# Performance work log

Measured on AMD Instinct MI355X. Metric: run time of the kernel, lower is better.

## Reference

```python
import jax, jax.numpy as jnp
import numpy as np

# ---- constants from the source module ----
N_SAMPLES = 2 ** 15          # exp.n_samples
N_FRAMES = 128
N_HARMONICS = 8
N_EVENTS = 8
FILT_SIZE = 16               # freq_domain_filter_size
N_NOTES = 128                # len(scale)
NYQ = 22050.0 / 2.0          # samplerate nyquist
MIN_F0 = 40.0 / NYQ
F0_SPAN = (3000.0 / NYQ) - MIN_F0
MIN_RES = 0.5
RES_SPAN = 1.0 - MIN_RES
B_EVENTS = 128               # batch(16) * n_events(8)

# packed layout (build_param_slices order):
SL_F0 = slice(0, N_NOTES)                       # 0:128
SL_AMP = slice(N_NOTES + N_FRAMES, N_NOTES + 2 * N_FRAMES)   # 256:384
SL_HAMP = slice(N_NOTES + 2 * N_FRAMES, N_NOTES + 2 * N_FRAMES + N_HARMONICS)  # 384:392
SL_HDEC = slice(N_NOTES + 2 * N_FRAMES + N_HARMONICS, N_NOTES + 2 * N_FRAMES + 2 * N_HARMONICS)  # 392:400
SL_FENV = slice(N_NOTES + 2 * N_FRAMES + 2 * N_HARMONICS, N_NOTES + 2 * N_FRAMES + 2 * N_HARMONICS + FILT_SIZE)  # 400:416


def interp_linear(x, out_size):
    """F.interpolate(..., mode='linear', align_corners=False) on last dim of [B,C,L]."""
    L = x.shape[-1]
    scale = L / out_size
    coords = (jnp.arange(out_size, dtype=x.dtype) + 0.5) * scale - 0.5
    coords = jnp.clip(coords, 0.0, L - 1)
    i0 = jnp.floor(coords).astype(jnp.int32)
    i1 = jnp.minimum(i0 + 1, L - 1)
    w = coords - i0.astype(x.dtype)
    return x[..., i0] * (1.0 - w) + x[..., i1] * w


def setup_inputs() -> dict:
    key = jax.random.key(0)
    k1, k2 = jax.random.split(key)
    packed = jax.random.uniform(k1, (B_EVENTS, N_NOTES + 2 * N_FRAMES + 2 * N_HARMONICS + FILT_SIZE), dtype=jnp.float32)
    # musical-scale center frequencies, normalized by nyquist (geometric 20..3000 Hz)
    hz = 20.0 * (3000.0 / 20.0) ** (np.arange(N_NOTES) / (N_NOTES - 1))
    frequencies = jnp.asarray(hz / NYQ, dtype=jnp.float32)
    global_amp = jnp.full((1,), 5000.0, dtype=jnp.float32)
    osc_amp = jnp.full((1,), 50.0, dtype=jnp.float32)
    noise = jax.random.uniform(k2, (B_EVENTS, 1, N_SAMPLES), dtype=jnp.float32, minval=-1.0, maxval=1.0)
    return {"packed": packed, "frequencies": frequencies, "global_amp": global_amp,
            "osc_amp": osc_amp, "noise": noise}


def reference(packed, frequencies, global_amp, osc_amp, noise):
    B = packed.shape[0]
    # ---- f0 (discrete): softmax over notes, expectation, squared, repeated per frame ----
    f0_scalar = jax.nn.softmax(packed[:, SL_F0], axis=-1) @ frequencies          # [B]
    f0 = (f0_scalar ** 2)[:, None, None] * jnp.ones((1, 1, N_FRAMES), packed.dtype)  # [B,1,F]
    f0 = f0 * NYQ
    f0 = MIN_F0 + f0 * F0_SPAN
    # (the torch line `f0 + f0 + f0_fine` has no assignment -> no effect; f0_fine unused)

    # ---- oscillator bank ----
    harm_factors = jnp.arange(1, N_HARMONICS + 1, dtype=packed.dtype)
    osc = f0 * harm_factors[None, :, None]                      # [B,H,F]
    radians = osc / NYQ * jnp.pi
    radians = jnp.where(radians >= jnp.pi, 0.0, radians)
    radians = interp_linear(radians, N_SAMPLES)                  # [B,H,S]
    osc_bank = jnp.sin(jnp.cumsum(radians, axis=-1)) * osc_amp   # [B,H,S]

    # ---- per-harmonic amplitude recurrence (scan over frames) ----
    harm_decay = MIN_RES + packed[:, SL_HDEC] * RES_SPAN         # [B,H]
    harm_amp = packed[:, SL_HAMP]                                # [B,H]
    amp = packed[:, SL_AMP][:, None, :] * 2.0 - 1.0              # [B,1,F]

    def step(current, amp_i):                                    # current [B,H], amp_i [B,1]
        cur = jnp.maximum(current + amp_i * harm_amp, 0.0)       # clamp(0, inf)
        return cur * harm_decay, cur

    amp_frames = jnp.moveaxis(amp[:, 0, :], 1, 0)[:, :, None]    # [F,B,1]
    _, res = jax.lax.scan(step, jnp.zeros((B, N_HARMONICS), packed.dtype), amp_frames)
    res = jnp.moveaxis(res, 0, 2)                                # [B,H,F]
    res_full = interp_linear(res, N_SAMPLES)                     # [B,H,S]

    # ---- FFT-filtered noise ----
    amp_full = interp_linear(amp, N_SAMPLES)                     # [B,1,S]
    nf = packed[:, SL_FENV][:, None, :]                          # [B,1,16]
    nf = interp_linear(nf, N_SAMPLES // 2)
    nf = jnp.pad(nf, ((0, 0), (0, 0), (0, 1)))                   # [B,1,S//2+1]
    noise_scaled = noise * global_amp
    spec = jnp.fft.rfft(noise_scaled, axis=-1, norm='ortho')
    filt = spec * nf
    noise_out = jnp.fft.irfft(filt, n=N_SAMPLES, axis=-1, norm='ortho')
    noise_out = noise_out * jnp.where(amp_full >= 0, amp_full, 0.2 * amp_full)  # leaky_relu(0.2)

    # ---- combine ----
    x = res_full * osc_bank                                      # [B,H,S]
    x = noise_out / N_HARMONICS + x                              # broadcast [B,1,S]
    x = x.reshape(-1, N_EVENTS, N_HARMONICS, N_SAMPLES)
    x = jnp.sum(x, axis=(1, 2)).reshape(-1, 1, N_SAMPLES)        # [batch,1,S]
    return x
```

## Files before the change

kernel.cpp:

```cpp
#include <hip/hip_runtime.h>
#include <math.h>

#define PCK_STRIDE 416
#define N_SAMPLES  32768
#define FFT_M      16384
#define B_EVENTS   128
#define N_GROUPS   16
#define NT         1024
#define PI_F 3.14159265358979323846f
#define RT2H 0.70710678118654752f

#define MAP(i) ((i) + (((i) >> 5) << 2))
#define LDS_N  18432

__device__ inline float filt_at(const float* __restrict__ f, int k) {
    if (k >= FFT_M) return 0.0f;
    float c = ((float)k + 0.5f) * (1.0f / 1024.0f) - 0.5f;
    c = fminf(fmaxf(c, 0.0f), 15.0f);
    int i0 = (int)floorf(c);
    int i1 = min(i0 + 1, 15);
    float w = c - (float)i0;
    return f[i0] * (1.0f - w) + f[i1] * w;
}

template<int L>
__device__ inline void r4_dif_stage(float* re, float* im, int tid) {
    constexpr int q = L >> 2;
    constexpr float ang = -6.28318530717958647692f / (float)L;
    #pragma unroll 1
    for (int s = 0; s < (FFT_M / 4) / NT; ++s) {
        int m = tid + s * NT;
        int t = m & (q - 1);
        int i0 = ((m & ~(q - 1)) << 2) | t;
        int ia = MAP(i0), ib = MAP(i0 + q), ic = MAP(i0 + 2 * q), id = MAP(i0 + 3 * q);
        float ar = re[ia], ai = im[ia];
        float br = re[ib], bi = im[ib];
        float cr = re[ic], ci = im[ic];
        float dr = re[id], di = im[id];
        float s1, c1; __sincosf(ang * (float)t, &s1, &c1);
        float c2 = c1 * c1 - s1 * s1, s2 = 2.0f * c1 * s1;
        float c3 = c2 * c1 - s2 * s1, s3 = c2 * s1 + s2 * c1;
        float s0r = ar + cr, s0i = ai + ci;
        float t1r = br + dr, t1i = bi + di;
        float d0r = ar - cr, d0i = ai - ci;
        float d1r = br - dr, d1i = bi - di;
        re[ia] = s0r + t1r; im[ia] = s0i + t1i;
        float er = s0r - t1r, ei = s0i - t1i;
        re[ib] = er * c2 - ei * s2; im[ib] = er * s2 + ei * c2;
        float fr = d0r + d1i, fi = d0i - d1r;
        re[ic] = fr * c1 - fi * s1; im[ic] = fr * s1 + fi * c1;
        float gr = d0r - d1i, gi = d0i + d1r;
        re[id] = gr * c3 - gi * s3; im[id] = gr * s3 + gi * c3;
    }
    __syncthreads();
}

template<int L>
__device__ inline void r4_dit_stage(float* re, float* im, int tid) {
    constexpr int q = L >> 2;
    constexpr float ang = 6.28318530717958647692f / (float)L;
    #pragma unroll 1
    for (int s = 0; s < (FFT_M / 4) / NT; ++s) {
        int m = tid + s * NT;
        int t = m & (q - 1);
        int i0 = ((m & ~(q - 1)) << 2) | t;
        int ia = MAP(i0), ib = MAP(i0 + q), ic = MAP(i0 + 2 * q), id = MAP(i0 + 3 * q);
        float ar = re[ia], ai = im[ia];
        float br = re[ib], bi = im[ib];
        float cr = re[ic], ci = im[ic];
        float dr = re[id], di = im[id];
        float s1, c1; __sincosf(ang * (float)t, &s1, &c1);
        float c2 = c1 * c1 - s1 * s1, s2 = 2.0f * c1 * s1;
        float tbr = br * c2 - bi * s2, tbi = br * s2 + bi * c2;
        float tdr = dr * c2 - di * s2, tdi = dr * s2 + di * c2;
        float B0r = ar + tbr, B0i = ai + tbi;
        float B1r = ar - tbr, B1i = ai - tbi;
        float B2r = cr + tdr, B2i = ci + tdi;
        float B3r = cr - tdr, B3i = ci - tdi;
        float t0r = B2r * c1 - B2i * s1, t0i = B2r * s1 + B2i * c1;
        float t1r = -B3r * s1 - B3i * c1, t1i = B3r * c1 - B3i * s1;
        re[ia] = B0r + t0r; im[ia] = B0i + t0i;
        re[ib] = B1r + t1r; im[ib] = B1i + t1i;
        re[ic] = B0r - t0r; im[ic] = B0i - t0i;
        re[id] = B1r - t1r; im[id] = B1i - t1i;
    }
    __syncthreads();
}

__global__ __launch_bounds__(NT)
void fft_filter_kernel(
    const float* __restrict__ noise, const float* __restrict__ packed,
    const float* __restrict__ gamp, float* __restrict__ noise_out,
    const float* __restrict__ freqs, float* __restrict__ rW, float* __restrict__ res)
{
    extern __shared__ float smem[];
    float* re = smem;
    float* im = smem + LDS_N;
    float* filt = smem + 2 * LDS_N;
    const int b = blockIdx.x;
    const int tid = threadIdx.x;
    const float g = gamp[0];

    const float2* nz = (const float2*)(noise + (size_t)b * N_SAMPLES);
    #pragma unroll 1
    for (int s = 0; s < 8192 / NT; ++s) {
        int j = tid + s * NT;
        float2 v0 = nz[j];
        float2 v1 = nz[j + 8192];
        float ur = v0.x * g, ui = v0.y * g;
        float wr = v1.x * g, wi = v1.y * g;
        float s1, c1; __sincosf((-PI_F / 8192.0f) * (float)j, &s1, &c1);
        int a0 = MAP(j), a1 = MAP(j + 8192);
        re[a0] = ur + wr; im[a0] = ui + wi;
        float dr = ur - wr, di = ui - wi;
        re[a1] = dr * c1 - di * s1;
        im[a1] = dr * s1 + di * c1;
    }
    if (tid >= 64 && tid < 80) filt[tid - 64] = packed[b * PCK_STRIDE + 400 + (tid - 64)];

    if (tid < 64) {
        const float* row = packed + b * PCK_STRIDE;
        float n0 = row[tid], n1 = row[tid + 64];
        float fq0 = freqs[tid], fq1 = freqs[tid + 64];
        float mx = fmaxf(n0, n1);
        #pragma unroll
        for (int off = 32; off >= 1; off >>= 1) mx = fmaxf(mx, __shfl_xor(mx, off));
        float e0 = __expf(n0 - mx), e1 = __expf(n1 - mx);
        float den = e0 + e1, num = e0 * fq0 + e1 * fq1;
        #pragma unroll
        for (int off = 32; off >= 1; off >>= 1) {
            den += __shfl_xor(den, off);
            num += __shfl_xor(num, off);
        }
        float ampA = row[256 + tid] * 2.0f - 1.0f;
        float ampB = row[320 + tid] * 2.0f - 1.0f;
        int h = tid & 7;
        float ha = row[384 + h];
        float hd = 0.5f + row[392 + h] * 0.5f;
        const float MIN_F0 = 40.0f / 11025.0f;
        const float F0_SPAN = 3000.0f / 11025.0f - 40.0f / 11025.0f;
        float f0s = num / den;
        float f0 = MIN_F0 + f0s * f0s * 11025.0f * F0_SPAN;
        float r = f0 * (float)(h + 1) * (PI_F / 11025.0f);
        if (r >= PI_F) r = 0.0f;
        if (tid < 8) rW[b * 8 + tid] = r;
        float cur = 0.0f;
        float* rr = res + (b * 8 + h) * 128;
        for (int f = 0; f < 64; ++f) {
            float av = __shfl(ampA, f);
            float c = fmaxf(cur + av * ha, 0.0f);
            if (tid < 8) rr[f] = c;
            cur = c * hd;
        }
        for (int f = 0; f < 64; ++f) {
            float av = __shfl(ampB, f);
            float c = fmaxf(cur + av * ha, 0.0f);
            if (tid < 8) rr[64 + f] = c;
            cur = c * hd;
        }
    }
    __syncthreads();

    r4_dif_stage<8192>(re, im, tid);
    r4_dif_stage<2048>(re, im, tid);
    r4_dif_stage<512>(re, im, tid);
    r4_dif_stage<128>(re, im, tid);
    r4_dif_stage<32>(re, im, tid);

    #pragma unroll 1
    for (int s = 0; s < 2048 / NT; ++s) {
        int m = (2048 / NT) * tid + s;
        int a = MAP(8 * m);
        float4 r0 = *(const float4*)(re + a);
        float4 r1 = *(const float4*)(re + a + 4);
        float4 q0 = *(const float4*)(im + a);
        float4 q1 = *(const float4*)(im + a + 4);
        float t0r = r0.x + r1.x, t0i = q0.x + q1.x;
        float u0r = r0.x - r1.x, u0i = q0.x - q1.x;
        float d1r = r0.y - r1.y, d1i = q0.y - q1.y;
        float t1r = r0.y + r1.y, t1i = q0.y + q1.y;
        float u1r = RT2H * (d1r + d1i), u1i = RT2H * (d1i - d1r);
        float t2r = r0.z + r1.z, t2i = q0.z + q1.z;
        float d2r = r0.z - r1.z, d2i = q0.z - q1.z;
        float u2r = d2i, u2i = -d2r;
        float t3r = r0.w + r1.w, t3i = q0.w + q1.w;
        float d3r = r0.w - r1.w, d3i = q0.w - q1.w;
        float u3r = RT2H * (d3i - d3r), u3i = -RT2H * (d3r + d3i);
        float A0r = t0r + t2r, A0i = t0i + t2i;
        float A2r = t0r - t2r, A2i = t0i - t2i;
        float A1r = t1r + t3r, A1i = t1i + t3i;
        float e3r = t1r - t3r, e3i = t1i - t3i;
        float A3r = e3i, A3i = -e3r;
        float B0r = u0r + u2r, B0i = u0i + u2i;
        float B2r = u0r - u2r, B2i = u0i - u2i;
        float B1r = u1r + u3r, B1i = u1i + u3i;
        float f3r = u1r - u3r, f3i = u1i - u3i;
        float B3r = f3i, B3i = -f3r;
        r0.x = A0r + A1r; q0.x = A0i + A1i;
        r0.y = A0r - A1r; q0.y = A0i - A1i;
        r0.z = A2r + A3r; q0.z = A2i + A3i;
        r0.w = A2r - A3r; q0.w = A2i - A3i;
        r1.x = B0r + B1r; q1.x = B0i + B1i;
        r1.y = B0r - B1r; q1.y = B0i - B1i;
        r1.z = B2r + B3r; q1.z = B2i + B3i;
        r1.w = B2r - B3r; q1.w = B2i - B3i;
        *(float4*)(re + a) = r0; *(float4*)(re + a + 4) = r1;
        *(float4*)(im + a) = q0; *(float4*)(im + a + 4) = q1;
    }
    __syncthreads();

    const float invM = 1.0f / (float)FFT_M;
    #pragma unroll 1
    for (int s = 0; s < 8192 / NT; ++s) {
        int jj = (tid + s * NT) << 1;
        if (jj == 0) {
            int p0 = MAP(0);
            float z0r = re[p0], z0i = im[p0];
            float y = 0.5f * filt_at(filt, 0) * (z0r + z0i) * invM;
            re[p0] = y; im[p0] = y;
            int p1 = MAP(1);
            float H = filt_at(filt, 8192) * invM;
            re[p1] *= H; im[p1] *= H;
        } else {
            int k = (int)(__brev((unsigned)jj) >> 18);
            int kq = FFT_M - k;
            int pk = MAP(jj);
            int pq = MAP((int)(__brev((unsigned)kq) >> 18));
            float zkr = re[pk], zki = im[pk];
            float zqr = re[pq], zqi = im[pq];
            float Er = 0.5f * (zkr + zqr), Ei = 0.5f * (zki - zqi);
            float Or = 0.5f * (zki + zqi), Oi = 0.5f * (zqr - zkr);
            float th = (float)k * (PI_F / (float)FFT_M);
            float s1, c1; __sincosf(th, &s1, &c1);
            float ts = -s1;
            float tOr = c1 * Or - ts * Oi;
            float tOi = c1 * Oi + ts * Or;
            float Hk = filt_at(filt, k);
            float Hq = filt_at(filt, kq);
            float Ykr = Hk * (Er + tOr), Yki = Hk * (Ei + tOi);
            float Cr  = Hq * (Er - tOr), Ci  = Hq * (Ei - tOi);
            float Ar = 0.5f * (Ykr + Cr), Ai = 0.5f * (Yki + Ci);
            float Br = 0.5f * (Ykr - Cr), Bi = 0.5f * (Yki - Ci);
            re[pk] = (Ar + ts * Br - c1 * Bi) * invM;
            im[pk] = (Ai + c1 * Br + ts * Bi) * invM;
            re[pq] = (Ar + c1 * Bi - ts * Br) * invM;
            im[pq] = (-Ai + c1 * Br + ts * Bi) * invM;
        }
    }
    __syncthreads();

    #pragma unroll 1
    for (int s = 0; s < 2048 / NT; ++s) {
        int m = (2048 / NT) * tid + s;
        int a = MAP(8 * m);
        float4 r0 = *(const float4*)(re + a);
        float4 r1 = *(const float4*)(re + a + 4);
        float4 q0 = *(const float4*)(im + a);
        float4 q1 = *(const float4*)(im + a + 4);
        float A0r = r0.x + r0.y, A0i = q0.x + q0.y;
        float A1r = r0.x - r0.y, A1i = q0.x - q0.y;
        float A2r = r0.z + r0.w, A2i = q0.z + q0.w;
        float A3r = r0.z - r0.w, A3i = q0.z - q0.w;
        float B0r = r1.x + r1.y, B0i = q1.x + q1.y;
        float B1r = r1.x - r1.y, B1i = q1.x - q1.y;
        float B2r = r1.z + r1.w, B2i = q1.z + q1.w;
        float B3r = r1.z - r1.w, B3i = q1.z - q1.w;
        float t0r = A0r + A2r, t0i = A0i + A2i;
        float t2r = A0r - A2r, t2i = A0i - A2i;
        float w3r = -A3i, w3i = A3r;
        float t1r = A1r + w3r, t1i = A1i + w3i;
        float t3r = A1r - w3r, t3i = A1i - w3i;
        float u0r = B0r + B2r, u0i = B0i + B2i;
        float u2r = B0r - B2r, u2i = B0i - B2i;
        float x3r = -B3i, x3i = B3r;
        float u1r = B1r + x3r, u1i = B1i + x3i;
        float u3r = B1r - x3r, u3i = B1i - x3i;
        float w1r = RT2H * (u1r - u1i), w1i = RT2H * (u1r + u1i);
        float w2r = -u2i,               w2i = u2r;
        float w5r = RT2H * (-u3r - u3i), w5i = RT2H * (u3r - u3i);
        r0.x = t0r + u0r; q0.x = t0i + u0i;
        r1.x = t0r - u0r; q1.x = t0i - u0i;
        r0.y = t1r + w1r; q0.y = t1i + w1i;
        r1.y = t1r - w1r; q1.y = t1i - w1i;
        r0.z = t2r + w2r; q0.z = t2i + w2i;
        r1.z = t2r - w2r; q1.z = t2i - w2i;
        r0.w = t3r + w5r; q0.w = t3i + w5i;
        r1.w = t3r - w5r; q1.w = t3i - w5i;
        *(float4*)(re + a) = r0; *(float4*)(re + a + 4) = r1;
        *(float4*)(im + a) = q0; *(float4*)(im + a + 4) = q1;
    }
    __syncthreads();

    r4_dit_stage<32>(re, im, tid);
    r4_dit_stage<128>(re, im, tid);
    r4_dit_stage<512>(re, im, tid);
    r4_dit_stage<2048>(re, im, tid);
    r4_dit_stage<8192>(re, im, tid);

    float2* oz = (float2*)(noise_out + (size_t)b * N_SAMPLES);
    #pragma unroll 1
    for (int s = 0; s < 8192 / NT; ++s) {
        int j = tid + s * NT;
        int a0 = MAP(j), a1 = MAP(j + 8192);
        float ur = re[a0], ui = im[a0];
        float xr = re[a1], xi = im[a1];
        float s1, c1; __sincosf((PI_F / 8192.0f) * (float)j, &s1, &c1);
        float wr = xr * c1 - xi * s1, wi = xr * s1 + xi * c1;
        oz[j] = make_float2(ur + wr, ui + wi);
        oz[j + 8192] = make_float2(ur - wr, ui - wi);
    }
}

__global__ __launch_bounds__(256) void assemble_kernel(
    const float* __restrict__ packed, const float* __restrict__ rW,
    const float* __restrict__ res, const float* __restrict__ noise_out,
    const float* __restrict__ oamp, float* __restrict__ out)
{
    const int g = blockIdx.y;
    const int chunk = blockIdx.x;
    const int tid = threadIdx.x;
    const int n = chunk * 256 + tid;
    const int fb = chunk - 1;

    __shared__ float s_res[8][8][3];
    __shared__ float s_ampf[8][3];
    __shared__ float s_r[8][8];
    if (tid < 192) {
        int e = tid / 24, rem = tid % 24, h = rem / 3, j = rem % 3;
        int f = min(max(fb + j, 0), 127);
        s_res[e][h][j] = res[((g * 8 + e) * 8 + h) * 128 + f];
    }
    if (tid < 24) {
        int e = tid / 3, j = tid % 3;
        int f = min(max(fb + j, 0), 127);
        s_ampf[e][j] = packed[(g * 8 + e) * PCK_STRIDE + 256 + f] * 2.0f - 1.0f;
    }
    if (tid >= 192 && tid < 256) {
        int u = tid - 192;
        s_r[u / 8][u % 8] = rW[g * 64 + u];
    }
    __syncthreads();

    float coords = ((float)n + 0.5f) * (1.0f / 256.0f) - 0.5f;
    coords = fminf(fmaxf(coords, 0.0f), 127.0f);
    int i0 = (int)floorf(coords);
    float w = coords - (float)i0;
    int j0 = i0 - fb;
    float osc50 = oamp[0];
    float pn = (float)(n + 1);
    float wm = 1.0f - w;

    float acc = 0.0f;
    #pragma unroll
    for (int e = 0; e < 8; ++e) {
        int b = g * 8 + e;
        float nv = noise_out[(size_t)b * N_SAMPLES + n];
        float av = s_ampf[e][j0] * wm + s_ampf[e][j0 + 1] * w;
        float gate = (av >= 0.0f) ? av : 0.2f * av;
        acc += nv * gate;
        float sn, cn; __sincosf(pn * s_r[e][0], &sn, &cn);
        float c2 = 2.0f * cn;
        float shm1 = 0.0f, sh = sn;
        #pragma unroll
        for (int h = 0; h < 8; ++h) {
            float rsv = s_res[e][h][j0] * wm + s_res[e][h][j0 + 1] * w;
            float sv = (s_r[e][h] != 0.0f) ? sh : 0.0f;
            acc += rsv * osc50 * sv;
            float nx = c2 * sh - shm1;
            shm1 = sh; sh = nx;
        }
    }
    out[(size_t)g * N_SAMPLES + n] = acc;
}

extern "C" void kernel_launch(void* const* d_in, const int* in_sizes, int n_in,
                              void* d_out, int out_size, void* d_ws, size_t ws_size,
                              hipStream_t stream) {
    const float* packed = (const float*)d_in[0];
    const float* freqs  = (const float*)d_in[1];
    const float* gamp   = (const float*)d_in[2];
    const float* oamp   = (const float*)d_in[3];
    const float* noise  = (const float*)d_in[4];
    float* out = (float*)d_out;

    float* ws = (float*)d_ws;
    float* noise_out = ws;
    float* res = ws + (size_t)B_EVENTS * N_SAMPLES;
    float* rW  = res + B_EVENTS * 8 * 128;

    fft_filter_kernel<<<B_EVENTS, NT, (2 * LDS_N + 16) * sizeof(float), stream>>>(
        noise, packed, gamp, noise_out, freqs, rW, res);
    assemble_kernel<<<dim3(N_SAMPLES / 256, N_GROUPS), 256, 0, stream>>>(
        packed, rW, res, noise_out, oamp, out);
}
```

Baseline: 116.8 us.

## Split each event's FFT into two independent half-size blocks, fuse final butterfly into assemble

The 16384-point complex FFT is decomposed by its first radix-2 DIF stage into two independent 8192-point halves, each processed by its own workgroup, doubling the grid to 256 blocks and halving LDS per block. The final inverse radix-2 recombination and twiddle are moved into the assemble kernel, which now reads both half-spectra and computes the output sample. This aims to fill more CUs and raise occupancy, at the cost of redundant noise loads per half and extra reads and sincos in assemble.

```diff
diff --git a/kernel.cpp b/kernel.cpp
--- a/kernel.cpp
+++ b/kernel.cpp
@@ -4,6 +4,7 @@
 #define PCK_STRIDE 416
 #define N_SAMPLES  32768
 #define FFT_M      16384
+#define HN         8192
 #define B_EVENTS   128
 #define N_GROUPS   16
 #define NT         1024
@@ -11,7 +12,7 @@
 #define RT2H 0.70710678118654752f
 
 #define MAP(i) ((i) + (((i) >> 5) << 2))
-#define LDS_N  18432
+#define LDS_H  9216
 
 __device__ inline float filt_at(const float* __restrict__ f, int k) {
     if (k >= FFT_M) return 0.0f;
@@ -28,7 +29,7 @@
     constexpr int q = L >> 2;
     constexpr float ang = -6.28318530717958647692f / (float)L;
     #pragma unroll 1
-    for (int s = 0; s < (FFT_M / 4) / NT; ++s) {
+    for (int s = 0; s < (HN / 4) / NT; ++s) {
         int m = tid + s * NT;
         int t = m & (q - 1);
         int i0 = ((m & ~(q - 1)) << 2) | t;
@@ -60,7 +61,7 @@
     constexpr int q = L >> 2;
     constexpr float ang = 6.28318530717958647692f / (float)L;
     #pragma unroll 1
-    for (int s = 0; s < (FFT_M / 4) / NT; ++s) {
+    for (int s = 0; s < (HN / 4) / NT; ++s) {
         int m = tid + s * NT;
         int t = m & (q - 1);
         int i0 = ((m & ~(q - 1)) << 2) | t;
@@ -88,37 +89,50 @@
 }
 
 __global__ __launch_bounds__(NT)
-void fft_filter_kernel(
+void fft_half_kernel(
     const float* __restrict__ noise, const float* __restrict__ packed,
-    const float* __restrict__ gamp, float* __restrict__ noise_out,
+    const float* __restrict__ gamp, float2* __restrict__ hd,
     const float* __restrict__ freqs, float* __restrict__ rW, float* __restrict__ res)
 {
     extern __shared__ float smem[];
     float* re = smem;
-    float* im = smem + LDS_N;
-    float* filt = smem + 2 * LDS_N;
-    const int b = blockIdx.x;
+    float* im = smem + LDS_H;
+    float* filt = smem + 2 * LDS_H;
+    const int half = blockIdx.x;
+    const int b = blockIdx.y;
     const int tid = threadIdx.x;
     const float g = gamp[0];
 
     const float2* nz = (const float2*)(noise + (size_t)b * N_SAMPLES);
-    #pragma unroll 1
-    for (int s = 0; s < 8192 / NT; ++s) {
-        int j = tid + s * NT;
-        float2 v0 = nz[j];
-        float2 v1 = nz[j + 8192];
-        float ur = v0.x * g, ui = v0.y * g;
-        float wr = v1.x * g, wi = v1.y * g;
-        float s1, c1; __sincosf((-PI_F / 8192.0f) * (float)j, &s1, &c1);
-        int a0 = MAP(j), a1 = MAP(j + 8192);
-        re[a0] = ur + wr; im[a0] = ui + wi;
-        float dr = ur - wr, di = ui - wi;
-        re[a1] = dr * c1 - di * s1;
-        im[a1] = dr * s1 + di * c1;
+    if (half == 0) {
+        #pragma unroll 1
+        for (int s = 0; s < HN / NT; ++s) {
+            int j = tid + s * NT;
+            float2 v0 = nz[j];
+            float2 v1 = nz[j + HN];
+            float ur = v0.x * g, ui = v0.y * g;
+            float wr = v1.x * g, wi = v1.y * g;
+            int a0 = MAP(j);
+            re[a0] = ur + wr; im[a0] = ui + wi;
+        }
+    } else {
+        #pragma unroll 1
+        for (int s = 0; s < HN / NT; ++s) {
+            int j = tid + s * NT;
+            float2 v0 = nz[j];
+            float2 v1 = nz[j + HN];
+            float ur = v0.x * g, ui = v0.y * g;
+            float wr = v1.x * g, wi = v1.y * g;
+            float dr = ur - wr, di = ui - wi;
+            float s1, c1; __sincosf((-PI_F / 8192.0f) * (float)j, &s1, &c1);
+            int a0 = MAP(j);
+            re[a0] = dr * c1 - di * s1;
+            im[a0] = dr * s1 + di * c1;
+        }
     }
     if (tid >= 64 && tid < 80) filt[tid - 64] = packed[b * PCK_STRIDE + 400 + (tid - 64)];
 
-    if (tid < 64) {
+    if (half == 0 && tid < 64) {
         const float* row = packed + b * PCK_STRIDE;
         float n0 = row[tid], n1 = row[tid + 64];
         float fq0 = freqs[tid], fq1 = freqs[tid + 64];
@@ -136,7 +150,7 @@
         float ampB = row[320 + tid] * 2.0f - 1.0f;
         int h = tid & 7;
         float ha = row[384 + h];
-        float hd = 0.5f + row[392 + h] * 0.5f;
+        float hdcy = 0.5f + row[392 + h] * 0.5f;
         const float MIN_F0 = 40.0f / 11025.0f;
         const float F0_SPAN = 3000.0f / 11025.0f - 40.0f / 11025.0f;
         float f0s = num / den;
@@ -150,13 +164,13 @@
             float av = __shfl(ampA, f);
             float c = fmaxf(cur + av * ha, 0.0f);
             if (tid < 8) rr[f] = c;
-            cur = c * hd;
+            cur = c * hdcy;
         }
         for (int f = 0; f < 64; ++f) {
             float av = __shfl(ampB, f);
             float c = fmaxf(cur + av * ha, 0.0f);
             if (tid < 8) rr[64 + f] = c;
-            cur = c * hd;
+            cur = c * hdcy;
         }
     }
     __syncthreads();
@@ -168,8 +182,8 @@
     r4_dif_stage<32>(re, im, tid);
 
     #pragma unroll 1
-    for (int s = 0; s < 2048 / NT; ++s) {
-        int m = (2048 / NT) * tid + s;
+    for (int s = 0; s < (HN / 8) / NT; ++s) {
+        int m = ((HN / 8) / NT) * tid + s;
         int a = MAP(8 * m);
         float4 r0 = *(const float4*)(re + a);
         float4 r1 = *(const float4*)(re + a + 4);
@@ -211,8 +225,9 @@
 
     const float invM = 1.0f / (float)FFT_M;
     #pragma unroll 1
-    for (int s = 0; s < 8192 / NT; ++s) {
-        int jj = (tid + s * NT) << 1;
+    for (int s = 0; s < (HN / 2) / NT; ++s) {
+        int p = (tid + s * NT) << 1;
+        int jj = (half << 13) | p;
         if (jj == 0) {
             int p0 = MAP(0);
             float z0r = re[p0], z0i = im[p0];
@@ -224,8 +239,8 @@
         } else {
             int k = (int)(__brev((unsigned)jj) >> 18);
             int kq = FFT_M - k;
-            int pk = MAP(jj);
-            int pq = MAP((int)(__brev((unsigned)kq) >> 18));
+            int pk = MAP(p);
+            int pq = MAP((int)(__brev((unsigned)kq) >> 18) & (HN - 1));
             float zkr = re[pk], zki = im[pk];
             float zqr = re[pq], zqi = im[pq];
             float Er = 0.5f * (zkr + zqr), Ei = 0.5f * (zki - zqi);
@@ -250,8 +265,8 @@
     __syncthreads();
 
     #pragma unroll 1
-    for (int s = 0; s < 2048 / NT; ++s) {
-        int m = (2048 / NT) * tid + s;
+    for (int s = 0; s < (HN / 8) / NT; ++s) {
+        int m = ((HN / 8) / NT) * tid + s;
         int a = MAP(8 * m);
         float4 r0 = *(const float4*)(re + a);
         float4 r1 = *(const float4*)(re + a + 4);
@@ -297,23 +312,17 @@
     r4_dit_stage<2048>(re, im, tid);
     r4_dit_stage<8192>(re, im, tid);
 
-    float2* oz = (float2*)(noise_out + (size_t)b * N_SAMPLES);
-    #pragma unroll 1
-    for (int s = 0; s < 8192 / NT; ++s) {
+    float2* dst = hd + (size_t)b * FFT_M + (half << 13);
+    #pragma unroll 1
+    for (int s = 0; s < HN / NT; ++s) {
         int j = tid + s * NT;
-        int a0 = MAP(j), a1 = MAP(j + 8192);
-        float ur = re[a0], ui = im[a0];
-        float xr = re[a1], xi = im[a1];
-        float s1, c1; __sincosf((PI_F / 8192.0f) * (float)j, &s1, &c1);
-        float wr = xr * c1 - xi * s1, wi = xr * s1 + xi * c1;
-        oz[j] = make_float2(ur + wr, ui + wi);
-        oz[j + 8192] = make_float2(ur - wr, ui - wi);
+        dst[j] = make_float2(re[MAP(j)], im[MAP(j)]);
     }
 }
 
 __global__ __launch_bounds__(256) void assemble_kernel(
     const float* __restrict__ packed, const float* __restrict__ rW,
-    const float* __restrict__ res, const float* __restrict__ noise_out,
+    const float* __restrict__ res, const float2* __restrict__ hd,
     const float* __restrict__ oamp, float* __restrict__ out)
 {
     const int g = blockIdx.y;
@@ -350,11 +359,23 @@
     float pn = (float)(n + 1);
     float wm = 1.0f - w;
 
+    const int jglob = n >> 1;
+    const int jl = jglob & (HN - 1);
+    const bool lo = (jglob < HN);
+    float sx, cx; __sincosf((PI_F / 8192.0f) * (float)jl, &sx, &cx);
+
     float acc = 0.0f;
     #pragma unroll
     for (int e = 0; e < 8; ++e) {
         int b = g * 8 + e;
-        float nv = noise_out[(size_t)b * N_SAMPLES + n];
+        const float2* hb = hd + (size_t)b * FFT_M;
+        float2 U = hb[jl];
+        float2 X = hb[jl + HN];
+        float wr2 = X.x * cx - X.y * sx;
+        float wi2 = X.x * sx + X.y * cx;
+        float nr = lo ? (U.x + wr2) : (U.x - wr2);
+        float ni = lo ? (U.y + wi2) : (U.y - wi2);
+        float nv = (n & 1) ? ni : nr;
         float av = s_ampf[e][j0] * wm + s_ampf[e][j0 + 1] * w;
         float gate = (av >= 0.0f) ? av : 0.2f * av;
         acc += nv * gate;
@@ -384,12 +405,12 @@
     float* out = (float*)d_out;
 
     float* ws = (float*)d_ws;
-    float* noise_out = ws;
+    float2* hd = (float2*)ws;
     float* res = ws + (size_t)B_EVENTS * N_SAMPLES;
     float* rW  = res + B_EVENTS * 8 * 128;
 
-    fft_filter_kernel<<<B_EVENTS, NT, (2 * LDS_N + 16) * sizeof(float), stream>>>(
-        noise, packed, gamp, noise_out, freqs, rW, res);
+    fft_half_kernel<<<dim3(2, B_EVENTS), NT, (2 * LDS_H + 16) * sizeof(float), stream>>>(
+        noise, packed, gamp, hd, freqs, rW, res);
     assemble_kernel<<<dim3(N_SAMPLES / 256, N_GROUPS), 256, 0, stream>>>(
-        packed, rW, res, noise_out, oamp, out);
-}
+        packed, rW, res, hd, oamp, out);
+}
```

After: 107.2 us. -8.3%, faster.
